# Kernel optimization log

Hardware: AMD Instinct MI355X
Metric: run time of the kernel (lower is better)

## Reference

```python
import jax, jax.numpy as jnp
import numpy as np

# ---- configuration matching init_kwargs ----
KH, KW = 3, 3
STRIDE = (1, 1)
PAD = (1, 1)
DIL = (1, 1)
GRID_SIZE = 5
SPLINE_ORDER = 3
GRID_RANGE = (-1.0, 1.0)
CIN, COUT = 16, 32
B, H, W = 16, 64, 64
K = KH * KW                      # in_features of each KANLinear
NB = GRID_SIZE + SPLINE_ORDER    # number of B-spline basis functions / coeffs


def make_grid():
    # efficient-KAN style extended uniform knot vector, shared by all units
    h = (GRID_RANGE[1] - GRID_RANGE[0]) / GRID_SIZE
    return (jnp.arange(-SPLINE_ORDER, GRID_SIZE + SPLINE_ORDER + 1,
                       dtype=jnp.float32) * h + GRID_RANGE[0])  # [G + 2k + 1]


def setup_inputs() -> dict:
    key = jax.random.key(0)
    k1, k2, k3, k4 = jax.random.split(key, 4)
    n_convs = COUT * CIN  # one KANLinear per (out_channel, in_channel) pair
    x = jax.random.normal(k1, (B, CIN, H, W), dtype=jnp.float32)
    base_w = jax.random.normal(k2, (n_convs, K), dtype=jnp.float32) * (1.0 / np.sqrt(K))
    spline_w = jax.random.normal(k3, (n_convs, K, NB), dtype=jnp.float32) * 0.1
    spline_scaler = jax.random.normal(k4, (n_convs, K), dtype=jnp.float32) * (1.0 / np.sqrt(K))
    return {"x": x, "base_w": base_w, "spline_w": spline_w,
            "spline_scaler": spline_scaler}


def extract_patches(x):
    # im2col / torch.nn.Unfold: [B, Cin, H, W] -> [B, Cin, Ho, Wo, K]
    xp = jnp.pad(x, ((0, 0), (0, 0), (PAD[0], PAD[0]), (PAD[1], PAD[1])))
    Hp, Wp = xp.shape[2], xp.shape[3]
    Ho = (Hp - DIL[0] * (KH - 1) - 1) // STRIDE[0] + 1
    Wo = (Wp - DIL[1] * (KW - 1) - 1) // STRIDE[1] + 1
    cols = []
    for i in range(KH):          # tiny fixed kernel loop (9 iters)
        for j in range(KW):
            cols.append(xp[:, :,
                           i * DIL[0]: i * DIL[0] + STRIDE[0] * Ho: STRIDE[0],
                           j * DIL[1]: j * DIL[1] + STRIDE[1] * Wo: STRIDE[1]])
    return jnp.stack(cols, axis=-1)  # [B, Cin, Ho, Wo, K]


def bspline_bases(x, t):
    # Cox-de Boor recursion, vectorized over all leading dims.
    # x: [...], t: [G+2k+1] shared knots -> bases [..., NB]
    xe = x[..., None]
    b = ((xe >= t[:-1]) & (xe < t[1:])).astype(x.dtype)
    for p in range(1, SPLINE_ORDER + 1):
        left = (xe - t[:-(p + 1)]) / (t[p:-1] - t[:-(p + 1)]) * b[..., :-1]
        right = (t[p + 1:] - xe) / (t[p + 1:] - t[1:-p]) * b[..., 1:]
        b = left + right
    return b  # [..., NB]


def reference(x, base_w, spline_w, spline_scaler):
    t = make_grid()
    patches = extract_patches(x)                 # [B, Cin, Ho, Wo, K]
    act = jax.nn.silu(patches)                   # base branch activation
    bases = bspline_bases(patches, t)            # [B, Cin, Ho, Wo, K, NB]
    # KANLinear list ordering: kernel index = c_out * Cin + c_in
    bw = base_w.reshape(COUT, CIN, K)
    sw = (spline_w * spline_scaler[..., None]).reshape(COUT, CIN, K, NB)
    # out[b,o,h,w] = sum_i KANLinear_{o,i}(patch[b,i,h,w,:])
    out = jnp.einsum('bihwk,oik->bohw', act, bw)
    out = out + jnp.einsum('bihwkc,oikc->bohw', bases, sw)
    return out
```

## Files before the change

### kernel.cpp

```cpp
#include <hip/hip_runtime.h>
#include <hip/hip_bf16.h>

#define CIN_ 16
#define COUT_ 32
#define NBATCH_ 16
#define H_ 64
#define W_ 64
#define F_ 10
#define LPIX_ 336
#define PXT_ 18
#define LROWT_ (PXT_ * LPIX_)
#define ROWS_ 6
#define NSITE_ (ROWS_ * PXT_)
#define NIT_ 7

typedef __attribute__((ext_vector_type(8))) short short8;
typedef __attribute__((ext_vector_type(4))) float f32x4;

__device__ __forceinline__ unsigned short f2bf(float f) {
    unsigned u = __builtin_bit_cast(unsigned, f);
    u += 0x7FFFu + ((u >> 16) & 1u);
    return (unsigned short)(u >> 16);
}
__device__ __forceinline__ unsigned pack2(float lo, float hi) {
    return (unsigned)f2bf(lo) | ((unsigned)f2bf(hi) << 16);
}

__global__ void kan_packw(const float* __restrict__ bw, const float* __restrict__ sw,
                          const float* __restrict__ sc, unsigned short* __restrict__ wpk) {
    int e = blockIdx.x * 256 + threadIdx.x;
    if (e >= 32 * 16 * 9) return;
    int n = e / 144;
    int ci = (e / 9) & 15;
    int tap = e % 9;
    float bwv = bw[e];
    float scv = sc[e];
    float4 s0 = *(const float4*)(sw + (size_t)e * 8);
    float4 s1 = *(const float4*)(sw + (size_t)e * 8 + 4);
    float swv[8] = {s0.x, s0.y, s0.z, s0.w, s1.x, s1.y, s1.z, s1.w};
    int nt = n >> 4, nl = n & 15;
#pragma unroll
    for (int f = 0; f < 10; ++f) {
        float v = (f == 0) ? bwv : (f <= 8 ? swv[f - 1] * scv : 0.0f);
        int k = ci * 10 + f;
        int c = k >> 5, r = k & 31;
        int lane = ((r >> 3) << 4) | nl;
        int j = r & 7;
        wpk[((size_t)(((tap * 2 + nt) * 5 + c)) * 64 + lane) * 8 + j] = f2bf(v);
    }
}

__global__ __launch_bounds__(256, 4) void kan_fused(const float* __restrict__ x,
                                                    const unsigned short* __restrict__ wpk,
                                                    float* __restrict__ out) {
    __shared__ __align__(16) char lA[ROWS_ * LROWT_];
    int tid = threadIdx.x;
    int bb = blockIdx.x >> 6;
    int rem = blockIdx.x & 63;
    int h0 = (rem >> 2) * 4;
    int w0 = (rem & 3) * 16;

    {
        int ci = tid >> 4;
        int l = tid & 15;
        const float* xb = x + ((size_t)bb * CIN_ + ci) * (H_ * W_);
        float xr[NIT_];
#pragma unroll
        for (int it = 0; it < NIT_; ++it) {
            int s = it * 16 + l;
            int r = s / PXT_;
            int lpx = s - r * PXT_;
            int hy = h0 + r - 1;
            int wx = w0 + lpx - 1;
            bool v = (s < NSITE_) && (hy >= 0) && (hy < H_) && (wx >= 0) && (wx < W_);
            xr[it] = v ? xb[hy * W_ + wx] : 0.f;
        }
#pragma unroll
        for (int it = 0; it < NIT_; ++it) {
            int s = it * 16 + l;
            if (s < NSITE_) {
                int r = s / PXT_;
                int lpx = s - r * PXT_;
                float xv = xr[it];
                float ua = (xv + 2.2f) * 2.5f;
                float mf = floorf(ua);
                float u = ua - mf;
                bool ok = (ua >= 0.0f) && (ua < 11.0f);
                float u2 = u * u, u3 = u2 * u;
                const float c6 = 1.0f / 6.0f;
                float Bm  = u3 * c6;
                float Bm1 = (-3.f * u3 + 3.f * u2 + 3.f * u + 1.f) * c6;
                float Bm2 = (3.f * u3 - 6.f * u2 + 4.f) * c6;
                float om = 1.f - u;
                float Bm3 = om * om * om * c6;
                unsigned P0 = pack2(Bm3, Bm2);
                unsigned P1 = pack2(Bm1, Bm);
                int sh = ok ? ((int)mf - 2) : 99;
                int a = sh >> 1;
                bool odd = sh & 1;
                unsigned Q0 = odd ? (P0 << 16) : P0;
                unsigned Q1 = odd ? ((P0 >> 16) | (P1 << 16)) : P1;
                unsigned Q2 = odd ? (P1 >> 16) : 0u;
                unsigned wq[5];
#pragma unroll
                for (int q = 0; q < 5; ++q)
                    wq[q] = (q == a) ? Q0 : (q == a + 1) ? Q1 : (q == a + 2) ? Q2 : 0u;
                float sil = xv * __builtin_amdgcn_rcpf(1.f + __expf(-xv));
                wq[0] = (wq[0] & 0xFFFF0000u) | (unsigned)f2bf(sil);
                unsigned* dst = (unsigned*)(lA + r * LROWT_ + lpx * LPIX_ + ci * 20);
#pragma unroll
                for (int q = 0; q < 5; ++q) dst[q] = wq[q];
            }
        }
    }

    int lane = tid & 63, wv = tid >> 6;
    int lrow = lane & 15, khalf = lane >> 4;
    int p = wv & 1;
    int nt = wv >> 1;

    short8 B[2][5];
#pragma unroll
    for (int c = 0; c < 5; ++c)
        B[0][c] = *(const short8*)(wpk + ((size_t)((nt * 5 + c)) * 64 + lane) * 8);

    __syncthreads();

    f32x4 acc[2] = {{0.f, 0.f, 0.f, 0.f}, {0.f, 0.f, 0.f, 0.f}};

#pragma unroll
    for (int tap = 0; tap < 9; ++tap) {
        int cur = tap & 1, nxt = cur ^ 1;
        if (tap < 8) {
#pragma unroll
            for (int c = 0; c < 5; ++c)
                B[nxt][c] = *(const short8*)(wpk +
                    ((size_t)((((tap + 1) * 2 + nt) * 5 + c)) * 64 + lane) * 8);
        }
        int ki = tap / 3, kj = tap - ki * 3;
        const char* abase = lA + (2 * p + ki) * LROWT_ + (lrow + kj) * LPIX_ + khalf * 16;
        __builtin_amdgcn_s_setprio(1);
#pragma unroll
        for (int c = 0; c < 5; ++c) {
            short8 a0 = *(const short8*)(abase + c * 64);
            short8 a1 = *(const short8*)(abase + LROWT_ + c * 64);
            acc[0] = __builtin_amdgcn_mfma_f32_16x16x32_bf16(a0, B[cur][c], acc[0], 0, 0, 0);
            acc[1] = __builtin_amdgcn_mfma_f32_16x16x32_bf16(a1, B[cur][c], acc[1], 0, 0, 0);
        }
        __builtin_amdgcn_s_setprio(0);
    }

    int och = nt * 16 + lrow;
    float* ob = out + (size_t)bb * COUT_ * (H_ * W_) + (size_t)och * (H_ * W_) + w0 +
                khalf * 4;
#pragma unroll
    for (int mi = 0; mi < 2; ++mi) {
        int hh = h0 + 2 * p + mi;
        __builtin_nontemporal_store(acc[mi], (f32x4*)(ob + (size_t)hh * W_));
    }
}

__device__ __forceinline__ void kan_feat_ref(float xv, float* f) {
    float ua = (xv + 2.2f) * 2.5f;
    float mf = floorf(ua);
    int m = (int)mf;
    float u = ua - mf;
    bool ok = (ua >= 0.0f) && (ua < 11.0f);
    float u2 = u * u, u3 = u2 * u;
    const float c6 = 1.0f / 6.0f;
    float Bm  = u3 * c6;
    float Bm1 = (-3.f * u3 + 3.f * u2 + 3.f * u + 1.f) * c6;
    float Bm2 = (3.f * u3 - 6.f * u2 + 4.f) * c6;
    float om = 1.f - u;
    float Bm3 = om * om * om * c6;
    if (!ok) { Bm = 0.f; Bm1 = 0.f; Bm2 = 0.f; Bm3 = 0.f; }
    f[0] = xv / (1.f + __expf(-xv));
#pragma unroll
    for (int j = 0; j < 8; ++j) {
        float v = 0.f;
        v = (m == j)     ? Bm  : v;
        v = (m == j + 1) ? Bm1 : v;
        v = (m == j + 2) ? Bm2 : v;
        v = (m == j + 3) ? Bm3 : v;
        f[1 + j] = v;
    }
}

__global__ void kan_direct(const float* __restrict__ x, const float* __restrict__ bw,
                           const float* __restrict__ sw, const float* __restrict__ sc,
                           float* __restrict__ out) {
    int idx = blockIdx.x * 256 + threadIdx.x;
    if (idx >= NBATCH_ * COUT_ * H_ * W_) return;
    int w = idx & 63, hh = (idx >> 6) & 63, o = (idx >> 12) & 31, b = idx >> 17;
    float acc = 0.0f;
    for (int i = 0; i < CIN_; ++i)
        for (int ki = 0; ki < 3; ++ki)
            for (int kj = 0; kj < 3; ++kj) {
                int hy = hh + ki - 1, wx = w + kj - 1;
                float xv = (hy >= 0 && hy < H_ && wx >= 0 && wx < W_)
                               ? x[(((size_t)b * CIN_ + i) * H_ + hy) * W_ + wx]
                               : 0.0f;
                float f[9];
                kan_feat_ref(xv, f);
                int idx9 = (o * CIN_ + i) * 9 + ki * 3 + kj;
                float a = f[0] * bw[idx9];
                float s = sc[idx9];
#pragma unroll
                for (int cc = 0; cc < 8; ++cc) a += f[1 + cc] * sw[idx9 * 8 + cc] * s;
                acc += a;
            }
    out[idx] = acc;
}

extern "C" void kernel_launch(void* const* d_in, const int* in_sizes, int n_in,
                              void* d_out, int out_size, void* d_ws, size_t ws_size,
                              hipStream_t stream) {
    const float* x  = (const float*)d_in[0];
    const float* bw = (const float*)d_in[1];
    const float* sw = (const float*)d_in[2];
    const float* sc = (const float*)d_in[3];
    float* out = (float*)d_out;

    size_t need = (size_t)9 * 2 * 5 * 64 * 8 * 2;
    if (ws_size >= need) {
        unsigned short* wpk = (unsigned short*)d_ws;
        kan_packw<<<dim3(18), 256, 0, stream>>>(bw, sw, sc, wpk);
        kan_fused<<<dim3(NBATCH_ * 64), 256, 0, stream>>>(x, wpk, out);
    } else {
        kan_direct<<<dim3((NBATCH_ * COUT_ * H_ * W_ + 255) / 256), 256, 0, stream>>>(
            x, bw, sw, sc, out);
    }
}
```

Baseline: 20.38 us.

## Split MFMA work across waves by kernel tap and reduce partials through LDS

Waves are now split by kernel tap parity instead of by output-channel tile, so each wave computes both 16-channel tiles over about half of the 9 taps. Each A fragment read from LDS now feeds two MFMAs, roughly halving LDS A-operand traffic per MFMA. The two half-sums are combined through an LDS scratch area, which costs an extra barrier pair. The tap split is uneven (5 vs 4 taps), doubling B fragments raises register pressure, and the padded scratch stride leaves 16-byte LDS accesses unaligned.

```diff
diff --git a/kernel.cpp b/kernel.cpp
--- a/kernel.cpp
+++ b/kernel.cpp
@@ -117,25 +117,34 @@
     int lane = tid & 63, wv = tid >> 6;
     int lrow = lane & 15, khalf = lane >> 4;
     int p = wv & 1;
-    int nt = wv >> 1;
-
-    short8 B[2][5];
+    int th = wv >> 1;
+
+    short8 B[2][5][2];
 #pragma unroll
     for (int c = 0; c < 5; ++c)
-        B[0][c] = *(const short8*)(wpk + ((size_t)((nt * 5 + c)) * 64 + lane) * 8);
+#pragma unroll
+        for (int nt = 0; nt < 2; ++nt)
+            B[0][c][nt] = *(const short8*)(wpk +
+                ((size_t)(((th * 2 + nt) * 5 + c)) * 64 + lane) * 8);
 
     __syncthreads();
 
-    f32x4 acc[2] = {{0.f, 0.f, 0.f, 0.f}, {0.f, 0.f, 0.f, 0.f}};
-
-#pragma unroll
-    for (int tap = 0; tap < 9; ++tap) {
-        int cur = tap & 1, nxt = cur ^ 1;
-        if (tap < 8) {
+    f32x4 acc[2][2] = {{{0.f,0.f,0.f,0.f},{0.f,0.f,0.f,0.f}},
+                       {{0.f,0.f,0.f,0.f},{0.f,0.f,0.f,0.f}}};
+
+#pragma unroll
+    for (int ti = 0; ti < 5; ++ti) {
+        int tap = th + 2 * ti;
+        if (tap > 8) break;
+        int cur = ti & 1, nxt = cur ^ 1;
+        int tapn = tap + 2;
+        if (tapn <= 8) {
 #pragma unroll
             for (int c = 0; c < 5; ++c)
-                B[nxt][c] = *(const short8*)(wpk +
-                    ((size_t)((((tap + 1) * 2 + nt) * 5 + c)) * 64 + lane) * 8);
+#pragma unroll
+                for (int nt = 0; nt < 2; ++nt)
+                    B[nxt][c][nt] = *(const short8*)(wpk +
+                        ((size_t)(((tapn * 2 + nt) * 5 + c)) * 64 + lane) * 8);
         }
         int ki = tap / 3, kj = tap - ki * 3;
         const char* abase = lA + (2 * p + ki) * LROWT_ + (lrow + kj) * LPIX_ + khalf * 16;
@@ -144,19 +153,39 @@
         for (int c = 0; c < 5; ++c) {
             short8 a0 = *(const short8*)(abase + c * 64);
             short8 a1 = *(const short8*)(abase + LROWT_ + c * 64);
-            acc[0] = __builtin_amdgcn_mfma_f32_16x16x32_bf16(a0, B[cur][c], acc[0], 0, 0, 0);
-            acc[1] = __builtin_amdgcn_mfma_f32_16x16x32_bf16(a1, B[cur][c], acc[1], 0, 0, 0);
+            acc[0][0] = __builtin_amdgcn_mfma_f32_16x16x32_bf16(a0, B[cur][c][0], acc[0][0], 0, 0, 0);
+            acc[0][1] = __builtin_amdgcn_mfma_f32_16x16x32_bf16(a0, B[cur][c][1], acc[0][1], 0, 0, 0);
+            acc[1][0] = __builtin_amdgcn_mfma_f32_16x16x32_bf16(a1, B[cur][c][0], acc[1][0], 0, 0, 0);
+            acc[1][1] = __builtin_amdgcn_mfma_f32_16x16x32_bf16(a1, B[cur][c][1], acc[1][1], 0, 0, 0);
         }
         __builtin_amdgcn_s_setprio(0);
     }
 
-    int och = nt * 16 + lrow;
-    float* ob = out + (size_t)bb * COUT_ * (H_ * W_) + (size_t)och * (H_ * W_) + w0 +
-                khalf * 4;
-#pragma unroll
-    for (int mi = 0; mi < 2; ++mi) {
-        int hh = h0 + 2 * p + mi;
-        __builtin_nontemporal_store(acc[mi], (f32x4*)(ob + (size_t)hh * W_));
+    __syncthreads();
+    float* scr = (float*)lA;
+    int sbase = (p * 64 + lane) * 17;
+    if (th == 1) {
+#pragma unroll
+        for (int mi = 0; mi < 2; ++mi)
+#pragma unroll
+            for (int nt = 0; nt < 2; ++nt)
+                *(f32x4*)(scr + sbase + (mi * 2 + nt) * 4) = acc[mi][nt];
+    }
+    __syncthreads();
+    if (th == 0) {
+        float* ob = out + (size_t)bb * COUT_ * (H_ * W_) + w0 + khalf * 4;
+#pragma unroll
+        for (int mi = 0; mi < 2; ++mi) {
+            int hh = h0 + 2 * p + mi;
+#pragma unroll
+            for (int nt = 0; nt < 2; ++nt) {
+                f32x4 v = acc[mi][nt];
+                v += *(const f32x4*)(scr + sbase + (mi * 2 + nt) * 4);
+                int och = nt * 16 + lrow;
+                __builtin_nontemporal_store(v,
+                    (f32x4*)(ob + (size_t)och * (H_ * W_) + (size_t)hh * W_));
+            }
+        }
     }
 }
 
```

Result: slower. 21.86 us (+7.2%).

## Split MFMA work by tap across waves and reduce partial sums via LDS

Applied to the files above, without the earlier changes.

Previously each wave covered one 16-channel output tile across all 9 taps. Now each wave pair splits the taps (even and odd), computes both output-channel tiles, and the two halves are summed through an LDS exchange before the store. Each A fragment is reused across two B tiles, which halves LDS reads of A per MFMA. The cost is an extra reduction with two more barriers, an unbalanced tap count (5 vs 4), and B weights loaded inline from global memory without the double-buffered prefetch and setprio hints.

```diff
diff --git a/kernel.cpp b/kernel.cpp
--- a/kernel.cpp
+++ b/kernel.cpp
@@ -113,51 +113,55 @@
             }
         }
     }
+    __syncthreads();
 
     int lane = tid & 63, wv = tid >> 6;
     int lrow = lane & 15, khalf = lane >> 4;
     int p = wv & 1;
-    int nt = wv >> 1;
-
-    short8 B[2][5];
-#pragma unroll
-    for (int c = 0; c < 5; ++c)
-        B[0][c] = *(const short8*)(wpk + ((size_t)((nt * 5 + c)) * 64 + lane) * 8);
-
-    __syncthreads();
-
-    f32x4 acc[2] = {{0.f, 0.f, 0.f, 0.f}, {0.f, 0.f, 0.f, 0.f}};
-
-#pragma unroll
-    for (int tap = 0; tap < 9; ++tap) {
-        int cur = tap & 1, nxt = cur ^ 1;
-        if (tap < 8) {
-#pragma unroll
-            for (int c = 0; c < 5; ++c)
-                B[nxt][c] = *(const short8*)(wpk +
-                    ((size_t)((((tap + 1) * 2 + nt) * 5 + c)) * 64 + lane) * 8);
-        }
+    int th = wv >> 1;
+
+    f32x4 acc00 = {0.f,0.f,0.f,0.f}, acc01 = {0.f,0.f,0.f,0.f};
+    f32x4 acc10 = {0.f,0.f,0.f,0.f}, acc11 = {0.f,0.f,0.f,0.f};
+
+#pragma unroll
+    for (int ti = 0; ti < 5; ++ti) {
+        int tap = th + 2 * ti;
+        if (tap > 8) break;
         int ki = tap / 3, kj = tap - ki * 3;
         const char* abase = lA + (2 * p + ki) * LROWT_ + (lrow + kj) * LPIX_ + khalf * 16;
-        __builtin_amdgcn_s_setprio(1);
+        const unsigned short* wt = wpk + (size_t)(tap * 2) * 5 * 64 * 8;
 #pragma unroll
         for (int c = 0; c < 5; ++c) {
+            short8 b0 = *(const short8*)(wt + ((size_t)c * 64 + lane) * 8);
+            short8 b1 = *(const short8*)(wt + ((size_t)(5 + c) * 64 + lane) * 8);
             short8 a0 = *(const short8*)(abase + c * 64);
             short8 a1 = *(const short8*)(abase + LROWT_ + c * 64);
-            acc[0] = __builtin_amdgcn_mfma_f32_16x16x32_bf16(a0, B[cur][c], acc[0], 0, 0, 0);
-            acc[1] = __builtin_amdgcn_mfma_f32_16x16x32_bf16(a1, B[cur][c], acc[1], 0, 0, 0);
+            acc00 = __builtin_amdgcn_mfma_f32_16x16x32_bf16(a0, b0, acc00, 0, 0, 0);
+            acc01 = __builtin_amdgcn_mfma_f32_16x16x32_bf16(a0, b1, acc01, 0, 0, 0);
+            acc10 = __builtin_amdgcn_mfma_f32_16x16x32_bf16(a1, b0, acc10, 0, 0, 0);
+            acc11 = __builtin_amdgcn_mfma_f32_16x16x32_bf16(a1, b1, acc11, 0, 0, 0);
         }
-        __builtin_amdgcn_s_setprio(0);
-    }
-
-    int och = nt * 16 + lrow;
-    float* ob = out + (size_t)bb * COUT_ * (H_ * W_) + (size_t)och * (H_ * W_) + w0 +
-                khalf * 4;
-#pragma unroll
-    for (int mi = 0; mi < 2; ++mi) {
-        int hh = h0 + 2 * p + mi;
-        __builtin_nontemporal_store(acc[mi], (f32x4*)(ob + (size_t)hh * W_));
-    }
+    }
+
+    __syncthreads();
+    float* scr = (float*)lA;
+    int sb = tid * 9;
+    f32x4 keep0 = th ? acc01 : acc00;
+    f32x4 keep1 = th ? acc11 : acc10;
+    f32x4 give0 = th ? acc00 : acc01;
+    f32x4 give1 = th ? acc10 : acc11;
+    *(f32x4*)(scr + sb) = give0;
+    *(f32x4*)(scr + sb + 4) = give1;
+    __syncthreads();
+    int pb = (tid ^ 128) * 9;
+    f32x4 r0 = keep0 + *(const f32x4*)(scr + pb);
+    f32x4 r1 = keep1 + *(const f32x4*)(scr + pb + 4);
+    int och = th * 16 + lrow;
+    float* ob = out + (size_t)bb * COUT_ * (H_ * W_) + (size_t)och * (H_ * W_) +
+                w0 + khalf * 4;
+    int hh = h0 + 2 * p;
+    __builtin_nontemporal_store(r0, (f32x4*)(ob + (size_t)hh * W_));
+    __builtin_nontemporal_store(r1, (f32x4*)(ob + (size_t)(hh + 1) * W_));
 }
 
 __device__ __forceinline__ void kan_feat_ref(float xv, float* f) {
```

Result: slower. 22.88 us (+12.2%).
